# Optimization experiments

Measured on AMD Instinct MI355X. Metric: run time of the kernel, lower is better.

The kernel has to match this reference:

```python
import jax, jax.numpy as jnp
from jax import lax
import numpy as np

B, A, D = 4, 512, 729   # batch, num_angles, detector pixels
H, W = 512, 512         # reconstruction volume


def setup_inputs() -> dict:
    key = jax.random.key(0)
    sino = jax.random.normal(key, (B, A, D), dtype=jnp.float32)
    vol_spacing = np.array([1.0, 1.0], dtype=np.float32)          # (sy, sx)
    det_spacing = np.array([1.0], dtype=np.float32)
    vol_origin = np.array([-(H - 1) / 2.0, -(W - 1) / 2.0], dtype=np.float32)
    det_origin = np.array([-(D - 1) / 2.0], dtype=np.float32)
    angles = jnp.linspace(0.0, jnp.pi, A, endpoint=False, dtype=jnp.float32)
    return {
        "input": sino,
        "volume_shape": np.array([H, W], dtype=np.int64),
        "volume_origin": jnp.asarray(vol_origin),
        "detector_origin": jnp.asarray(det_origin),
        "volume_spacing": jnpp if False else jnp.asarray(vol_spacing),
        "detector_spacing": jnp.asarray(det_spacing),
        "trajectory": angles,
    }


def _backproject(sino, vol_shape, vol_origin, det_origin, vol_spacing, det_spacing, angles):
    h, w = int(vol_shape[0]), int(vol_shape[1])
    d = sino.shape[-1]
    ys = vol_origin[0] + jnp.arange(h, dtype=sino.dtype) * vol_spacing[0]  # [H]
    xs = vol_origin[1] + jnp.arange(w, dtype=sino.dtype) * vol_spacing[1]  # [W]

    def step(acc, per_angle):
        theta, sino_a = per_angle                      # scalar, [B, D]
        # ray coordinate s = x*cos(theta) + y*sin(theta) for every voxel
        s = xs[None, :] * jnp.cos(theta) + ys[:, None] * jnp.sin(theta)  # [H, W]
        u = (s - det_origin[0]) / det_spacing[0]       # continuous detector index
        u0 = jnp.floor(u)
        frac = u - u0
        i0 = u0.astype(jnp.int32)
        i1 = i0 + 1
        valid0 = (i0 >= 0) & (i0 < d)
        valid1 = (i1 >= 0) & (i1 < d)
        i0c = jnp.clip(i0, 0, d - 1)
        i1c = jnp.clip(i1, 0, d - 1)
        v0 = sino_a[:, i0c]                            # [B, H, W] gather
        v1 = sino_a[:, i1c]                            # [B, H, W] gather
        contrib = (jnp.where(valid0, (1.0 - frac) * v0, 0.0)
                   + jnp.where(valid1, frac * v1, 0.0))
        return acc + contrib, None

    acc0 = jnp.zeros((sino.shape[0], h, w), dtype=sino.dtype)
    out, _ = lax.scan(step, acc0, (angles, jnp.swapaxes(sino, 0, 1)))
    return out


def reference(input, volume_shape, volume_origin, detector_origin,
              volume_spacing, detector_spacing, trajectory):
    return _backproject(input, volume_shape, volume_origin, detector_origin,
                        volume_spacing, detector_spacing, trajectory)
```

## Files before the change

kernel.cpp:

```cpp
#include <hip/hip_runtime.h>

#define BB 4
#define AA 512
#define ZS 4
#define AH (AA / ZS)
#define DD 729
#define HH 512
#define WW 512
#define CH 16
#define WIN 32

typedef float f4v __attribute__((ext_vector_type(4)));

__device__ inline void gload_lds(const float* g, float* l) {
    __builtin_amdgcn_global_load_lds(
        (const __attribute__((address_space(1))) unsigned int*)g,
        (__attribute__((address_space(3))) unsigned int*)l, 4, 0, 0);
}

__global__ __launch_bounds__(128, 8) void bp_kernel(
    const float* __restrict__ sino,
    const float* __restrict__ vol_origin,
    const float* __restrict__ det_origin,
    const float* __restrict__ vol_spacing,
    const float* __restrict__ det_spacing,
    const float* __restrict__ angles,
    float* __restrict__ out)
{
    __shared__ f4v   s_csk[AH];
    __shared__ int   s_s0[AH];
    __shared__ float s_win[CH * WIN * BB];

    const int tid  = threadIdx.y * 16 + threadIdx.x;
    const int lane = tid & 63;
    const int wv   = tid >> 6;

    const float inv_ds = 1.0f / det_spacing[0];
    const int abase = blockIdx.z * AH;

    const int x0 = blockIdx.x * 16;
    const int y0 = blockIdx.y * 16;
    const float vsx = vol_spacing[1], vsy = vol_spacing[0];
    const float off = -det_origin[0] * inv_ds;
    const float xc = vol_origin[1] + ((float)x0 + 7.5f) * vsx;
    const float yc = vol_origin[0] + ((float)y0 + 7.5f) * vsy;

    for (int a = tid; a < AH; a += 128) {
        float th = angles[abase + a];
        float c = cosf(th) * inv_ds;
        float s = sinf(th) * inv_ds;
        float uc = fmaf(xc, c, fmaf(yc, s, off));
        int s0 = min(max((int)uc - (WIN / 2), 0), DD - WIN);
        f4v k;
        k.x = c; k.y = s; k.z = off - (float)s0; k.w = 8.0f * vsy * s;
        s_csk[a] = k;
        s_s0[a]  = s0;
    }
    __syncthreads();

    const int ix  = x0 + threadIdx.x;
    const int iyA = y0 + threadIdx.y;
    const float xw = vol_origin[1] + (float)ix * vsx;
    const float yw = vol_origin[0] + (float)iyA * vsy;

    const int sidx = wv * 64 + lane;
    const int se   = sidx >> 2;
    const int sbb  = lane & 3;
    const long sgoff = (long)sbb * (AA * DD) + se;

    f4v accA = {0.f, 0.f, 0.f, 0.f};
    f4v accB = {0.f, 0.f, 0.f, 0.f};

    for (int a0 = 0; a0 < AH; a0 += CH) {
        #pragma unroll
        for (int i = 0; i < CH; ++i) {
            const int  s0  = s_s0[a0 + i];
            const long row = (long)(abase + a0 + i) * DD + s0;
            gload_lds(sino + row + sgoff, &s_win[i * (WIN * BB) + wv * 64]);
        }
        __syncthreads();

        #pragma unroll
        for (int j = 0; j < CH; ++j) {
            const f4v  k  = s_csk[a0 + j];
            const float u0 = fmaf(xw, k.x, fmaf(yw, k.y, k.z));
            const float u1 = u0 + k.w;
            {
                const int   li = (int)u0;
                const float fr = __builtin_amdgcn_fractf(u0);
                const f4v* w = (const f4v*)&s_win[(j * WIN + li) * BB];
                const f4v P = w[0], Q = w[1];
                const f4v fr4 = {fr, fr, fr, fr};
                accA = accA + P + fr4 * (Q - P);
            }
            {
                const int   li = (int)u1;
                const float fr = __builtin_amdgcn_fractf(u1);
                const f4v* w = (const f4v*)&s_win[(j * WIN + li) * BB];
                const f4v P = w[0], Q = w[1];
                const f4v fr4 = {fr, fr, fr, fr};
                accB = accB + P + fr4 * (Q - P);
            }
        }
        __syncthreads();
    }

    const size_t HW = (size_t)HH * WW;
    const size_t oA = (size_t)iyA * WW + ix;
    const size_t oB = oA + (size_t)8 * WW;
    unsafeAtomicAdd(&out[oA],          accA.x);
    unsafeAtomicAdd(&out[oA + HW],     accA.y);
    unsafeAtomicAdd(&out[oA + 2 * HW], accA.z);
    unsafeAtomicAdd(&out[oA + 3 * HW], accA.w);
    unsafeAtomicAdd(&out[oB],          accB.x);
    unsafeAtomicAdd(&out[oB + HW],     accB.y);
    unsafeAtomicAdd(&out[oB + 2 * HW], accB.z);
    unsafeAtomicAdd(&out[oB + 3 * HW], accB.w);
}

extern "C" void kernel_launch(void* const* d_in, const int* in_sizes, int n_in,
                              void* d_out, int out_size, void* d_ws, size_t ws_size,
                              hipStream_t stream) {
    const float* sino        = (const float*)d_in[0];
    const float* vol_origin  = (const float*)d_in[2];
    const float* det_origin  = (const float*)d_in[3];
    const float* vol_spacing = (const float*)d_in[4];
    const float* det_spacing = (const float*)d_in[5];
    const float* angles      = (const float*)d_in[6];
    float* out = (float*)d_out;

    hipMemsetAsync(d_out, 0, (size_t)out_size * sizeof(float), stream);

    dim3 block(16, 8, 1);
    dim3 grid(WW / 16, HH / 16, ZS);
    bp_kernel<<<grid, block, 0, stream>>>(sino, vol_origin, det_origin,
                                          vol_spacing, det_spacing, angles, out);
}
```

Before: 142.8 us.

## Double-buffer sinogram window loads and restructure lerp as two FMAs

Splits the LDS sinogram window into two buffers of half the chunk size and issues the async global-to-LDS loads for the next chunk before computing on the current one, removing one barrier per iteration. The goal is to overlap global load latency with the interpolation math. It also rewrites the lerp as fr*Q + (1-fr)*P so it maps to FMAs. The risk is that the async LDS loads may not be waited on correctly with a single barrier, and the lerp rewrite adds a subtraction per sample.

```diff
diff --git a/kernel.cpp b/kernel.cpp
--- a/kernel.cpp
+++ b/kernel.cpp
@@ -7,7 +7,7 @@
 #define DD 729
 #define HH 512
 #define WW 512
-#define CH 16
+#define CH 8
 #define WIN 32
 
 typedef float f4v __attribute__((ext_vector_type(4)));
@@ -29,7 +29,7 @@
 {
     __shared__ f4v   s_csk[AH];
     __shared__ int   s_s0[AH];
-    __shared__ float s_win[CH * WIN * BB];
+    __shared__ float s_win[2][CH * WIN * BB];
 
     const int tid  = threadIdx.y * 16 + threadIdx.x;
     const int lane = tid & 63;
@@ -64,22 +64,27 @@
     const float yw = vol_origin[0] + (float)iyA * vsy;
 
     const int sidx = wv * 64 + lane;
-    const int se   = sidx >> 2;
-    const int sbb  = lane & 3;
-    const long sgoff = (long)sbb * (AA * DD) + se;
+    const long sgoff = (long)(lane & 3) * (AA * DD) + (sidx >> 2);
 
     f4v accA = {0.f, 0.f, 0.f, 0.f};
     f4v accB = {0.f, 0.f, 0.f, 0.f};
 
+    #define STAGE(A0, P)                                                   \
+        do {                                                               \
+            _Pragma("unroll")                                              \
+            for (int i = 0; i < CH; ++i) {                                 \
+                const int  s0  = s_s0[(A0) + i];                           \
+                const long row = (long)(abase + (A0) + i) * DD + s0;       \
+                gload_lds(sino + row + sgoff,                              \
+                          &s_win[P][i * (WIN * BB) + wv * 64]);            \
+            }                                                              \
+        } while (0)
+
+    int p = 0;
+    STAGE(0, 0);
     for (int a0 = 0; a0 < AH; a0 += CH) {
-        #pragma unroll
-        for (int i = 0; i < CH; ++i) {
-            const int  s0  = s_s0[a0 + i];
-            const long row = (long)(abase + a0 + i) * DD + s0;
-            gload_lds(sino + row + sgoff, &s_win[i * (WIN * BB) + wv * 64]);
-        }
         __syncthreads();
-
+        if (a0 + CH < AH) STAGE(a0 + CH, p ^ 1);
         #pragma unroll
         for (int j = 0; j < CH; ++j) {
             const f4v  k  = s_csk[a0 + j];
@@ -88,22 +93,27 @@
             {
                 const int   li = (int)u0;
                 const float fr = __builtin_amdgcn_fractf(u0);
-                const f4v* w = (const f4v*)&s_win[(j * WIN + li) * BB];
+                const float om = 1.0f - fr;
+                const f4v* w = (const f4v*)&s_win[p][(j * WIN + li) * BB];
                 const f4v P = w[0], Q = w[1];
                 const f4v fr4 = {fr, fr, fr, fr};
-                accA = accA + P + fr4 * (Q - P);
+                const f4v om4 = {om, om, om, om};
+                accA = accA + fr4 * Q + om4 * P;
             }
             {
                 const int   li = (int)u1;
                 const float fr = __builtin_amdgcn_fractf(u1);
-                const f4v* w = (const f4v*)&s_win[(j * WIN + li) * BB];
+                const float om = 1.0f - fr;
+                const f4v* w = (const f4v*)&s_win[p][(j * WIN + li) * BB];
                 const f4v P = w[0], Q = w[1];
                 const f4v fr4 = {fr, fr, fr, fr};
-                accB = accB + P + fr4 * (Q - P);
+                const f4v om4 = {om, om, om, om};
+                accB = accB + fr4 * Q + om4 * P;
             }
         }
-        __syncthreads();
+        p ^= 1;
     }
+    #undef STAGE
 
     const size_t HW = (size_t)HH * WW;
     const size_t oA = (size_t)iyA * WW + ix;
```

New measurement: 136.2 us. -4.6%, faster.
